# Performance work log

Hardware: AMD Instinct MI355X
Metric: run time of the kernel (lower is better)

Reference implementation:

```python
import jax, jax.numpy as jnp
import numpy as np
from jax import lax

B, CIN, H, W = 16, 256, 64, 64
DP = 512          # displace_planes
COUT = 256        # outplanes
NUM_OFFSET = 64   # displace_planes // BIND_CHAN(8)
K = 5             # DPOOL_SIZE (odd)
EPS = float(np.finfo(np.float32).eps)
BN_EPS = 1e-5
EXP_CLAMP = 88.722835


def conv1x1(x, w, b):
    # x: [B,C,H,W], w: [O,C], b: [O]
    return jnp.einsum('bchw,oc->bohw', x, w) + b[None, :, None, None]


def batchnorm(x, gamma, beta):
    m = x.mean(axis=(0, 2, 3))
    v = x.var(axis=(0, 2, 3))
    inv = lax.rsqrt(v + BN_EPS)
    return (x - m[None, :, None, None]) * (inv * gamma)[None, :, None, None] + beta[None, :, None, None]


def dynamic_pool(x, sigma):
    # per-channel Gaussian depthwise conv in exp space, back to log space
    r = (jnp.arange(K) - K // 2).astype(jnp.float32)
    dissq = r[:, None] ** 2 + r[None, :] ** 2                     # [K,K]
    kern = jnp.exp(-(dissq / 2.0)[None] / (sigma ** 2 + EPS)[:, None, None])  # [C,K,K]
    kern = kern / kern.sum(axis=(1, 2), keepdims=True)
    expx = jnp.exp(jnp.minimum(x, EXP_CLAMP))
    out = lax.conv_general_dilated(
        expx, kern[:, None],                                      # rhs [C,1,K,K]
        window_strides=(1, 1), padding=[(K // 2, K // 2)] * 2,
        dimension_numbers=('NCHW', 'OIHW', 'NCHW'),
        feature_group_count=DP)
    return jnp.log(out + EPS)


def displace(feat, offsets):
    # feat: [B,C,H,W]; offsets: [NUM_OFFSET,2] (dy,dx), each bound to C//NUM_OFFSET channels.
    # Per-channel uniform bilinear shift with zero padding outside the map.
    Bn, C, Hn, Wn = feat.shape
    chan = C // NUM_OFFSET
    dy = jnp.repeat(offsets[:, 0], chan)  # [C]
    dx = jnp.repeat(offsets[:, 1], chan)
    y0 = jnp.floor(dy); x0 = jnp.floor(dx)
    fy = dy - y0; fx = dx - x0            # fractional parts (diff. wrt offsets)
    y0i = y0.astype(jnp.int32); x0i = x0.astype(jnp.int32)
    rows = jnp.arange(Hn); cols = jnp.arange(Wn)

    def one_chan(img, y0c, x0c, fyc, fxc):
        # img: [B,H,W]; shift is separable per row/col since offset is uniform
        def shifted(oy, ox):
            ry = rows + y0c + oy
            rx = cols + x0c + ox
            my = (ry >= 0) & (ry < Hn)
            mx = (rx >= 0) & (rx < Wn)
            g = img[:, jnp.clip(ry, 0, Hn - 1), :][:, :, jnp.clip(rx, 0, Wn - 1)]
            return g * (my[:, None] & mx[None, :]).astype(img.dtype)[None]
        return ((1 - fyc) * (1 - fxc) * shifted(0, 0)
                + (1 - fyc) * fxc * shifted(0, 1)
                + fyc * (1 - fxc) * shifted(1, 0)
                + fyc * fxc * shifted(1, 1))

    return jax.vmap(one_chan, in_axes=(1, 0, 0, 0, 0), out_axes=1)(feat, y0i, x0i, fy, fx)


def attention(x, w, b, gamma, beta):
    a = conv1x1(x, w, b)
    a = batchnorm(a, gamma, beta)
    a = jax.nn.softplus(a)
    # SpaceNormalization: normalize over spatial dims
    return a / a.sum(axis=(2, 3), keepdims=True)


def setup_inputs() -> dict:
    key = jax.random.key(0)
    ks = jax.random.split(key, 6)
    return {
        'x': jax.random.normal(ks[0], (B, CIN, H, W), jnp.float32),
        'pre_w': jax.random.normal(ks[1], (DP, CIN), jnp.float32) / np.sqrt(CIN),
        'pre_b': jnp.zeros((DP,), jnp.float32),
        'sigma': jnp.full((DP,), K / 2 / 2, jnp.float32),
        'offsets': jax.random.normal(ks[2], (NUM_OFFSET, 2), jnp.float32) * 3.0,
        'atten_w': jax.random.normal(ks[3], (DP, CIN), jnp.float32) / np.sqrt(CIN),
        'atten_b': jnp.zeros((DP,), jnp.float32),
        'atten_gamma': jnp.ones((DP,), jnp.float32),
        'atten_beta': jnp.zeros((DP,), jnp.float32),
        'post_w': jax.random.normal(ks[4], (COUT, DP), jnp.float32) / np.sqrt(DP),
        'post_b': jnp.zeros((COUT,), jnp.float32),
        'bn_gamma': jnp.ones((COUT,), jnp.float32),
        'bn_beta': jnp.zeros((COUT,), jnp.float32),
    }


def reference(x, pre_w, pre_b, sigma, offsets, atten_w, atten_b, atten_gamma,
              atten_beta, post_w, post_b, bn_gamma, bn_beta):
    out_pre = conv1x1(x, pre_w, pre_b)                 # [B,DP,H,W]
    out_pre = dynamic_pool(out_pre, sigma)
    out_dis = displace(out_pre, offsets)
    out_atten = attention(x, atten_w, atten_b, atten_gamma, atten_beta)
    out_post = conv1x1(out_atten * out_dis, post_w, post_b)  # [B,COUT,H,W]
    out_skip = x + out_post                            # inplanes==outplanes, stride=1
    return jax.nn.relu(batchnorm(out_skip, bn_gamma, bn_beta))
```

## Files before the change

kernel.cpp:

```cpp
#include <hip/hip_runtime.h>
#include <cmath>

#define NB   16
#define CINC 256
#define DPC  512
#define COUTC 256
#define HWS  4096
#define EPSF 1.1920928955078125e-07f
#define BN_EPS 1e-5f
#define EXP_CLAMP 88.722835f
#define TS 76
#define PS2 66

typedef unsigned int uint32;
typedef unsigned short ushort;
typedef __bf16 bf16x8 __attribute__((ext_vector_type(8)));
typedef float f32x4 __attribute__((ext_vector_type(4)));
typedef unsigned short ushort8 __attribute__((ext_vector_type(8)));

__device__ inline ushort f2bf(float f) {
    __bf16 h = (__bf16)f;
    return __builtin_bit_cast(ushort, h);
}
__device__ inline float bf2f(ushort u) {
    return __builtin_bit_cast(float, (uint32)u << 16);
}
__device__ inline float softplus_fast(float v) {
    return fmaxf(v, 0.f) + __logf(1.f + __expf(-fabsf(v)));
}
__device__ __forceinline__ void gload16(const void* g, void* l) {
    __builtin_amdgcn_global_load_lds(
        (__attribute__((address_space(1))) void*)g,
        (__attribute__((address_space(3))) void*)l, 16, 0, 0);
}

template<int OTOT, int KTOT, bool BF16_OUT, bool ADD_SKIP>
__global__ __launch_bounds__(256) void mfma_gemm_k(
    const ushort* __restrict__ A, const ushort* __restrict__ BT,
    const float* __restrict__ bias1, const float* __restrict__ bias2,
    const float* __restrict__ skip, void* __restrict__ outv) {
    const int hw0 = blockIdx.x * 128;
    const int o0  = blockIdx.y * 128;
    const int b   = blockIdx.z;
    __shared__ ushort As[2 * 128 * 32];
    __shared__ ushort Bs[2 * 128 * 32];
    const int tid  = threadIdx.x;
    const int lane = tid & 63;
    const int w    = tid >> 6;
    const int wm0  = (w >> 1) * 64;
    const int wn0  = (w & 1) * 64;

    f32x4 acc[4][4] = {};

    const ushort* Ab = A + (size_t)o0 * KTOT;
    const ushort* Bb = BT + ((size_t)b * HWS + hw0) * KTOT;
    const int rsub  = lane >> 2;
    const int ksubp = ((lane & 3) ^ ((lane >> 3) & 3)) * 8;

    for (int step = 0; step < KTOT / 64; ++step) {
        const int k0 = step * 64;
#pragma unroll
        for (int h = 0; h < 2; ++h)
#pragma unroll
            for (int i = 0; i < 2; ++i) {
                const int row = w * 32 + i * 16 + rsub;
                gload16(Ab + (size_t)row * KTOT + k0 + h * 32 + ksubp,
                        &As[h * 4096 + (w * 32 + i * 16) * 32]);
                gload16(Bb + (size_t)row * KTOT + k0 + h * 32 + ksubp,
                        &Bs[h * 4096 + (w * 32 + i * 16) * 32]);
            }
        __syncthreads();
        bf16x8 af[2][4], bfr[2][4];
#pragma unroll
        for (int h = 0; h < 2; ++h) {
#pragma unroll
            for (int mi = 0; mi < 4; ++mi) {
                int row = wm0 + mi * 16 + (lane & 15);
                int sl = (lane >> 4) ^ ((row >> 1) & 3);
                af[h][mi] = *reinterpret_cast<const bf16x8*>(As + h * 4096 + row * 32 + sl * 8);
            }
#pragma unroll
            for (int ni = 0; ni < 4; ++ni) {
                int row = wn0 + ni * 16 + (lane & 15);
                int sl = (lane >> 4) ^ ((row >> 1) & 3);
                bfr[h][ni] = *reinterpret_cast<const bf16x8*>(Bs + h * 4096 + row * 32 + sl * 8);
            }
        }
#pragma unroll
        for (int h = 0; h < 2; ++h)
#pragma unroll
            for (int mi = 0; mi < 4; ++mi)
#pragma unroll
                for (int ni = 0; ni < 4; ++ni)
                    acc[mi][ni] = __builtin_amdgcn_mfma_f32_16x16x32_bf16(
                        af[h][mi], bfr[h][ni], acc[mi][ni], 0, 0, 0);
        __syncthreads();
    }

#pragma unroll
    for (int mi = 0; mi < 4; ++mi) {
#pragma unroll
        for (int r = 0; r < 4; ++r) {
            int o = o0 + wm0 + mi * 16 + ((lane >> 4) << 2) + r;
            float bi = (o < 512) ? bias1[o] : bias2[o - 512];
            size_t base = ((size_t)b * OTOT + o) * HWS + hw0 + wn0 + (lane & 15);
            if constexpr (BF16_OUT) {
                ushort* outp = (ushort*)outv;
#pragma unroll
                for (int ni = 0; ni < 4; ++ni)
                    outp[base + ni * 16] = f2bf(acc[mi][ni][r] + bi);
            } else {
                float* outp = (float*)outv;
#pragma unroll
                for (int ni = 0; ni < 4; ++ni) {
                    float v = acc[mi][ni][r] + bi;
                    if constexpr (ADD_SKIP) v += skip[base + ni * 16];
                    outp[base + ni * 16] = v;
                }
            }
        }
    }
}

__global__ __launch_bounds__(256) void castT_k(const float* __restrict__ x,
                                               ushort* __restrict__ xT) {
    const int b = blockIdx.z, c0 = blockIdx.y * 64, hw0 = blockIdx.x * 64;
    __shared__ float tile[64][65];
    const int tid = threadIdx.x;
#pragma unroll
    for (int r = 0; r < 16; ++r) {
        int cl = r * 4 + (tid >> 6), hwl = tid & 63;
        tile[cl][hwl] = x[((size_t)b * CINC + c0 + cl) * HWS + hw0 + hwl];
    }
    __syncthreads();
#pragma unroll
    for (int r = 0; r < 16; ++r) {
        int hwl = r * 4 + (tid >> 6), cl = tid & 63;
        xT[((size_t)b * HWS + hw0 + hwl) * CINC + c0 + cl] = f2bf(tile[cl][hwl]);
    }
}

__global__ __launch_bounds__(256) void cast_k(const float* __restrict__ in,
                                              ushort* __restrict__ out, int n) {
    int i = (blockIdx.x * 256 + threadIdx.x) * 4;
    if (i < n) {
        float4 v = *reinterpret_cast<const float4*>(in + i);
        out[i + 0] = f2bf(v.x); out[i + 1] = f2bf(v.y);
        out[i + 2] = f2bf(v.z); out[i + 3] = f2bf(v.w);
    }
}

__global__ __launch_bounds__(512, 8) void pooldisp_k(ushort* __restrict__ dp,
                                                     const float* __restrict__ sigma,
                                                     const float* __restrict__ offsets) {
    const int bc = blockIdx.x;
    const int b = bc >> 9, c = bc & 511;
    __shared__ float  tmp[68 * TS];
    __shared__ ushort pl[64 * PS2];
    const int tid = threadIdx.x;
    ushort* ip = dp + ((size_t)b * 1024 + c) * HWS;

    float s = sigma[c];
    float inv = 0.5f / (s * s + EPSF);
    float g0 = __expf(-4.f * inv), g1 = __expf(-1.f * inv);
    float gs = g0 + g1 + 1.f + g1 + g0;
    float rnorm = 1.f / (gs * gs);

    {
        int r4 = tid >> 7, col = tid & 127;
        if (col < TS) {
            int row = (r4 < 2) ? r4 : 64 + r4;
            tmp[row * TS + col] = 0.f;
        }
    }
    {
        int hr = tid >> 3, w0 = (tid & 7) * 8;
        const ushort* rp = ip + hr * 64 + w0;
        ushort8 mv = *reinterpret_cast<const ushort8*>(rp);
        float e[12];
        e[0] = (w0 > 0) ? __expf(fminf(bf2f(rp[-2]), EXP_CLAMP)) : 0.f;
        e[1] = (w0 > 0) ? __expf(fminf(bf2f(rp[-1]), EXP_CLAMP)) : 0.f;
#pragma unroll
        for (int q = 0; q < 8; ++q)
            e[2 + q] = __expf(fminf(bf2f(mv[q]), EXP_CLAMP));
        e[10] = (w0 < 56) ? __expf(fminf(bf2f(rp[8]), EXP_CLAMP)) : 0.f;
        e[11] = (w0 < 56) ? __expf(fminf(bf2f(rp[9]), EXP_CLAMP)) : 0.f;
        f32x4 o0, o1;
#pragma unroll
        for (int j = 0; j < 4; ++j) {
            o0[j] = g0 * (e[j] + e[j + 4]) + g1 * (e[j + 1] + e[j + 3]) + e[j + 2];
            o1[j] = g0 * (e[j + 4] + e[j + 8]) + g1 * (e[j + 5] + e[j + 7]) + e[j + 6];
        }
        *reinterpret_cast<f32x4*>(&tmp[(hr + 2) * TS + w0]) = o0;
        *reinterpret_cast<f32x4*>(&tmp[(hr + 2) * TS + w0 + 4]) = o1;
    }
    __syncthreads();

#pragma unroll
    for (int t = 0; t < 2; ++t) {
        int task = tid + t * 512;
        int h = task >> 4, wq = (task & 15) * 4;
        f32x4 t0 = *reinterpret_cast<const f32x4*>(&tmp[(h + 0) * TS + wq]);
        f32x4 t1 = *reinterpret_cast<const f32x4*>(&tmp[(h + 1) * TS + wq]);
        f32x4 t2 = *reinterpret_cast<const f32x4*>(&tmp[(h + 2) * TS + wq]);
        f32x4 t3 = *reinterpret_cast<const f32x4*>(&tmp[(h + 3) * TS + wq]);
        f32x4 t4 = *reinterpret_cast<const f32x4*>(&tmp[(h + 4) * TS + wq]);
        ushort o[4];
#pragma unroll
        for (int j = 0; j < 4; ++j) {
            float v = g0 * (t0[j] + t4[j]) + g1 * (t1[j] + t3[j]) + t2[j];
            o[j] = f2bf(__logf(v * rnorm + EPSF));
        }
        *reinterpret_cast<uint32*>(&pl[h * PS2 + wq]) =
            (uint32)o[0] | ((uint32)o[1] << 16);
        *reinterpret_cast<uint32*>(&pl[h * PS2 + wq + 2]) =
            (uint32)o[2] | ((uint32)o[3] << 16);
    }
    __syncthreads();

    {
        int oi = c >> 3;
        float dy = offsets[oi * 2 + 0];
        float dx = offsets[oi * 2 + 1];
        float y0f = floorf(dy), x0f = floorf(dx);
        float fy = dy - y0f, fx = dx - x0f;
        int y0 = (int)y0f, x0 = (int)x0f;
        float w00 = (1.f - fy) * (1.f - fx), w01 = (1.f - fy) * fx;
        float w10 = fy * (1.f - fx),         w11 = fy * fx;
        int h = tid >> 3, w = (tid & 7) * 8;
        int ry0 = h + y0, ry1 = ry0 + 1;
        bool my0 = (ry0 >= 0) & (ry0 < 64);
        bool my1 = (ry1 >= 0) & (ry1 < 64);
        float e0[9], e1[9];
#pragma unroll
        for (int j = 0; j < 9; ++j) {
            int col = w + x0 + j;
            bool mx = (col >= 0) & (col < 64);
            e0[j] = (my0 & mx) ? bf2f(pl[ry0 * PS2 + col]) : 0.f;
            e1[j] = (my1 & mx) ? bf2f(pl[ry1 * PS2 + col]) : 0.f;
        }
        ushort8 ov;
#pragma unroll
        for (int q = 0; q < 8; ++q)
            ov[q] = f2bf(w00 * e0[q] + w01 * e0[q + 1]
                       + w10 * e1[q] + w11 * e1[q + 1]);
        *reinterpret_cast<ushort8*>(ip + tid * 8) = ov;
    }
}

__global__ __launch_bounds__(1024) void attstats_k(const ushort* __restrict__ dp,
                                                   const float* __restrict__ gamma,
                                                   const float* __restrict__ beta,
                                                   float* __restrict__ scale,
                                                   float* __restrict__ shift,
                                                   float* __restrict__ rsum) {
    const int c = blockIdx.x;
    const int t = threadIdx.x;
    const int wv = t >> 6, lane = t & 63;
    const ushort* p = dp + ((size_t)wv * 1024 + 512 + c) * HWS;

    ushort8 v[8];
    float s = 0.f, s2 = 0.f;
#pragma unroll
    for (int k = 0; k < 8; ++k) {
        v[k] = *reinterpret_cast<const ushort8*>(p + lane * 8 + k * 512);
#pragma unroll
        for (int j = 0; j < 8; ++j) { float f = bf2f(v[k][j]); s += f; s2 += f * f; }
    }
#pragma unroll
    for (int off = 32; off > 0; off >>= 1) {
        s += __shfl_down(s, off, 64);
        s2 += __shfl_down(s2, off, 64);
    }
    __shared__ float t1[16], t2[16], scsh[2];
    if (lane == 0) { t1[wv] = s; t2[wv] = s2; }
    __syncthreads();
    if (t == 0) {
        float S = 0.f, S2 = 0.f;
#pragma unroll
        for (int k = 0; k < 16; ++k) { S += t1[k]; S2 += t2[k]; }
        float n = (float)(NB * HWS);
        float mean = S / n;
        float var = S2 / n - mean * mean;
        float invs = rsqrtf(var + BN_EPS);
        float sc = invs * gamma[c];
        float sh = beta[c] - mean * sc;
        scale[c] = sc; shift[c] = sh;
        scsh[0] = sc; scsh[1] = sh;
    }
    __syncthreads();
    float sc = scsh[0], sh = scsh[1];
    float ps = 0.f;
#pragma unroll
    for (int k = 0; k < 8; ++k)
#pragma unroll
        for (int j = 0; j < 8; ++j)
            ps += softplus_fast(bf2f(v[k][j]) * sc + sh);
#pragma unroll
    for (int off = 32; off > 0; off >>= 1) ps += __shfl_down(ps, off, 64);
    if (lane == 0) rsum[wv * DPC + c] = 1.f / ps;
}

__global__ __launch_bounds__(256) void attmulT_k(const ushort* __restrict__ dp,
                                                 const float* __restrict__ scale,
                                                 const float* __restrict__ shift,
                                                 const float* __restrict__ rsum,
                                                 ushort* __restrict__ mT) {
    const int b = blockIdx.z, c0 = blockIdx.y * 64, hw0 = blockIdx.x * 64;
    __shared__ float tile[64][65];
    const int tid = threadIdx.x;
#pragma unroll
    for (int r = 0; r < 16; ++r) {
        int cl = r * 4 + (tid >> 6), hwl = tid & 63;
        int c = c0 + cl;
        size_t aidx = ((size_t)b * 1024 + 512 + c) * HWS + hw0 + hwl;
        size_t didx = ((size_t)b * 1024 + c) * HWS + hw0 + hwl;
        float a = bf2f(dp[aidx]) * scale[c] + shift[c];
        float m = softplus_fast(a) * rsum[b * DPC + c] * bf2f(dp[didx]);
        tile[cl][hwl] = m;
    }
    __syncthreads();
#pragma unroll
    for (int r = 0; r < 16; ++r) {
        int hwl = r * 4 + (tid >> 6), cl = tid & 63;
        mT[((size_t)b * HWS + hw0 + hwl) * DPC + c0 + cl] = f2bf(tile[cl][hwl]);
    }
}

__global__ __launch_bounds__(1024) void bnstats_k(const float* __restrict__ a,
                                                  const float* __restrict__ gamma,
                                                  const float* __restrict__ beta,
                                                  float* __restrict__ scale,
                                                  float* __restrict__ shift) {
    const int c = blockIdx.x;
    const int t = threadIdx.x;
    const int wv = t >> 6, lane = t & 63;
    const float* p = a + ((size_t)wv * COUTC + c) * HWS;
    float s = 0.f, s2 = 0.f;
#pragma unroll
    for (int k = 0; k < 16; ++k) {
        float4 v = *reinterpret_cast<const float4*>(p + lane * 4 + k * 256);
        s += v.x + v.y + v.z + v.w;
        s2 += v.x * v.x + v.y * v.y + v.z * v.z + v.w * v.w;
    }
#pragma unroll
    for (int off = 32; off > 0; off >>= 1) {
        s += __shfl_down(s, off, 64);
        s2 += __shfl_down(s2, off, 64);
    }
    __shared__ float t1[16], t2[16];
    if (lane == 0) { t1[wv] = s; t2[wv] = s2; }
    __syncthreads();
    if (t == 0) {
        float S = 0.f, S2 = 0.f;
#pragma unroll
        for (int k = 0; k < 16; ++k) { S += t1[k]; S2 += t2[k]; }
        float n = (float)(NB * HWS);
        float mean = S / n;
        float var = S2 / n - mean * mean;
        float invs = rsqrtf(var + BN_EPS);
        float sc = invs * gamma[c];
        scale[c] = sc;
        shift[c] = beta[c] - mean * sc;
    }
}

__global__ __launch_bounds__(256) void final_k(float* __restrict__ out,
                                               const float* __restrict__ scale,
                                               const float* __restrict__ shift) {
    int i = blockIdx.x * 256 + threadIdx.x;
    int c = (i >> 12) & (COUTC - 1);
    float v = out[i] * scale[c] + shift[c];
    out[i] = fmaxf(v, 0.f);
}

extern "C" void kernel_launch(void* const* d_in, const int* in_sizes, int n_in,
                              void* d_out, int out_size, void* d_ws, size_t ws_size,
                              hipStream_t stream) {
    const float* x           = (const float*)d_in[0];
    const float* pre_w       = (const float*)d_in[1];
    const float* pre_b       = (const float*)d_in[2];
    const float* sigma       = (const float*)d_in[3];
    const float* offsets     = (const float*)d_in[4];
    const float* atten_w     = (const float*)d_in[5];
    const float* atten_b     = (const float*)d_in[6];
    const float* atten_gamma = (const float*)d_in[7];
    const float* atten_beta  = (const float*)d_in[8];
    const float* post_w      = (const float*)d_in[9];
    const float* post_b      = (const float*)d_in[10];
    const float* bn_gamma    = (const float*)d_in[11];
    const float* bn_beta     = (const float*)d_in[12];
    float* out = (float*)d_out;

    char* wsb = (char*)d_ws;
    ushort* xT    = (ushort*)(wsb);
    ushort* wbig  = (ushort*)(wsb + ((size_t)32 << 20));
    ushort* wpost = wbig + 1024 * 256;
    float*  stats = (float*)(wsb + ((size_t)33 << 20));
    ushort* dpout = (ushort*)(wsb + ((size_t)34 << 20));
    ushort* mT    = (ushort*)(wsb + ((size_t)162 << 20));

    float* scaleA = stats;
    float* shiftA = stats + 512;
    float* rsum   = stats + 1024;
    float* scale2 = stats + 9216;
    float* shift2 = stats + 9472;

    castT_k<<<dim3(64, 4, NB), 256, 0, stream>>>(x, xT);
    cast_k<<<128, 256, 0, stream>>>(pre_w,   wbig,             DPC * CINC);
    cast_k<<<128, 256, 0, stream>>>(atten_w, wbig + 512 * 256, DPC * CINC);
    cast_k<<<128, 256, 0, stream>>>(post_w,  wpost,            COUTC * DPC);

    mfma_gemm_k<1024, CINC, true, false><<<dim3(32, 8, NB), 256, 0, stream>>>(
        wbig, xT, pre_b, atten_b, nullptr, dpout);
    pooldisp_k<<<NB * DPC, 512, 0, stream>>>(dpout, sigma, offsets);
    attstats_k<<<DPC, 1024, 0, stream>>>(dpout, atten_gamma, atten_beta,
                                         scaleA, shiftA, rsum);
    attmulT_k<<<dim3(64, 8, NB), 256, 0, stream>>>(dpout, scaleA, shiftA, rsum, mT);
    mfma_gemm_k<COUTC, DPC, false, true><<<dim3(32, 2, NB), 256, 0, stream>>>(
        wpost, mT, post_b, post_b, x, out);
    bnstats_k<<<COUTC, 1024, 0, stream>>>(out, bn_gamma, bn_beta, scale2, shift2);
    final_k<<<out_size / 256, 256, 0, stream>>>(out, scale2, shift2);
}
```

Baseline: 288.1 us.

## Fuse BN statistics into post GEMM epilogue and store bf16 intermediate

Result: faster. 276.6 us (-4.0%).

```diff
diff --git a/kernel.cpp b/kernel.cpp
--- a/kernel.cpp
+++ b/kernel.cpp
@@ -34,16 +34,17 @@
         (__attribute__((address_space(3))) void*)l, 16, 0, 0);
 }
 
-template<int OTOT, int KTOT, bool BF16_OUT, bool ADD_SKIP>
+template<int OTOT, int KTOT, bool DUALBIAS, bool PARTIALS>
 __global__ __launch_bounds__(256) void mfma_gemm_k(
     const ushort* __restrict__ A, const ushort* __restrict__ BT,
     const float* __restrict__ bias1, const float* __restrict__ bias2,
-    const float* __restrict__ skip, void* __restrict__ outv) {
+    const float* __restrict__ skip, ushort* __restrict__ outp,
+    float* __restrict__ part_s, float* __restrict__ part_s2) {
     const int hw0 = blockIdx.x * 128;
     const int o0  = blockIdx.y * 128;
     const int b   = blockIdx.z;
-    __shared__ ushort As[2 * 128 * 32];
-    __shared__ ushort Bs[2 * 128 * 32];
+    __shared__ ushort As[2][128 * 32];
+    __shared__ ushort Bs[2][128 * 32];
     const int tid  = threadIdx.x;
     const int lane = tid & 63;
     const int w    = tid >> 6;
@@ -57,67 +58,90 @@
     const int rsub  = lane >> 2;
     const int ksubp = ((lane & 3) ^ ((lane >> 3) & 3)) * 8;
 
-    for (int step = 0; step < KTOT / 64; ++step) {
-        const int k0 = step * 64;
-#pragma unroll
-        for (int h = 0; h < 2; ++h)
-#pragma unroll
-            for (int i = 0; i < 2; ++i) {
-                const int row = w * 32 + i * 16 + rsub;
-                gload16(Ab + (size_t)row * KTOT + k0 + h * 32 + ksubp,
-                        &As[h * 4096 + (w * 32 + i * 16) * 32]);
-                gload16(Bb + (size_t)row * KTOT + k0 + h * 32 + ksubp,
-                        &Bs[h * 4096 + (w * 32 + i * 16) * 32]);
-            }
+    auto stage = [&](int buf, int k0) {
+#pragma unroll
+        for (int i = 0; i < 2; ++i) {
+            const int row = w * 32 + i * 16 + rsub;
+            gload16(Ab + (size_t)row * KTOT + k0 + ksubp, &As[buf][(w * 32 + i * 16) * 32]);
+            gload16(Bb + (size_t)row * KTOT + k0 + ksubp, &Bs[buf][(w * 32 + i * 16) * 32]);
+        }
+    };
+
+    constexpr int NSTEP = KTOT / 32;
+    stage(0, 0);
+    __syncthreads();
+    int cur = 0;
+    for (int step = 0; step < NSTEP; ++step) {
+        if (step + 1 < NSTEP) stage(cur ^ 1, (step + 1) * 32);
+        bf16x8 af[4], bfr[4];
+#pragma unroll
+        for (int mi = 0; mi < 4; ++mi) {
+            int row = wm0 + mi * 16 + (lane & 15);
+            int sl = (lane >> 4) ^ ((row >> 1) & 3);
+            af[mi] = *reinterpret_cast<const bf16x8*>(&As[cur][row * 32 + sl * 8]);
+        }
+#pragma unroll
+        for (int ni = 0; ni < 4; ++ni) {
+            int row = wn0 + ni * 16 + (lane & 15);
+            int sl = (lane >> 4) ^ ((row >> 1) & 3);
+            bfr[ni] = *reinterpret_cast<const bf16x8*>(&Bs[cur][row * 32 + sl * 8]);
+        }
+#pragma unroll
+        for (int mi = 0; mi < 4; ++mi)
+#pragma unroll
+            for (int ni = 0; ni < 4; ++ni)
+                acc[mi][ni] = __builtin_amdgcn_mfma_f32_16x16x32_bf16(
+                    af[mi], bfr[ni], acc[mi][ni], 0, 0, 0);
         __syncthreads();
-        bf16x8 af[2][4], bfr[2][4];
-#pragma unroll
-        for (int h = 0; h < 2; ++h) {
-#pragma unroll
-            for (int mi = 0; mi < 4; ++mi) {
-                int row = wm0 + mi * 16 + (lane & 15);
-                int sl = (lane >> 4) ^ ((row >> 1) & 3);
-                af[h][mi] = *reinterpret_cast<const bf16x8*>(As + h * 4096 + row * 32 + sl * 8);
-            }
+        cur ^= 1;
+    }
+
+    float* pS  = reinterpret_cast<float*>(&As[0][0]);
+    float* pS2 = pS + 256;
+
+#pragma unroll
+    for (int mi = 0; mi < 4; ++mi) {
+#pragma unroll
+        for (int r = 0; r < 4; ++r) {
+            int chL = wm0 + mi * 16 + ((lane >> 4) << 2) + r;
+            int o = o0 + chL;
+            float bi;
+            if constexpr (DUALBIAS) bi = (o < 512) ? bias1[o] : bias2[o - 512];
+            else bi = bias1[o];
+            size_t base = ((size_t)b * OTOT + o) * HWS + hw0 + wn0 + (lane & 15);
+            float s1 = 0.f, s2 = 0.f;
 #pragma unroll
             for (int ni = 0; ni < 4; ++ni) {
-                int row = wn0 + ni * 16 + (lane & 15);
-                int sl = (lane >> 4) ^ ((row >> 1) & 3);
-                bfr[h][ni] = *reinterpret_cast<const bf16x8*>(Bs + h * 4096 + row * 32 + sl * 8);
-            }
-        }
-#pragma unroll
-        for (int h = 0; h < 2; ++h)
-#pragma unroll
-            for (int mi = 0; mi < 4; ++mi)
-#pragma unroll
-                for (int ni = 0; ni < 4; ++ni)
-                    acc[mi][ni] = __builtin_amdgcn_mfma_f32_16x16x32_bf16(
-                        af[h][mi], bfr[h][ni], acc[mi][ni], 0, 0, 0);
-        __syncthreads();
-    }
-
-#pragma unroll
-    for (int mi = 0; mi < 4; ++mi) {
-#pragma unroll
-        for (int r = 0; r < 4; ++r) {
-            int o = o0 + wm0 + mi * 16 + ((lane >> 4) << 2) + r;
-            float bi = (o < 512) ? bias1[o] : bias2[o - 512];
-            size_t base = ((size_t)b * OTOT + o) * HWS + hw0 + wn0 + (lane & 15);
-            if constexpr (BF16_OUT) {
-                ushort* outp = (ushort*)outv;
-#pragma unroll
-                for (int ni = 0; ni < 4; ++ni)
-                    outp[base + ni * 16] = f2bf(acc[mi][ni][r] + bi);
-            } else {
-                float* outp = (float*)outv;
-#pragma unroll
-                for (int ni = 0; ni < 4; ++ni) {
-                    float v = acc[mi][ni][r] + bi;
-                    if constexpr (ADD_SKIP) v += skip[base + ni * 16];
-                    outp[base + ni * 16] = v;
+                float v = acc[mi][ni][r] + bi;
+                if constexpr (PARTIALS) v += skip[base + ni * 16];
+                ushort tb = f2bf(v);
+                outp[base + ni * 16] = tb;
+                if constexpr (PARTIALS) {
+                    float vf = bf2f(tb);
+                    s1 += vf; s2 += vf * vf;
                 }
             }
+            if constexpr (PARTIALS) {
+#pragma unroll
+                for (int off = 1; off <= 8; off <<= 1) {
+                    s1 += __shfl_xor(s1, off, 64);
+                    s2 += __shfl_xor(s2, off, 64);
+                }
+                if ((lane & 15) == 0) {
+                    pS[(w & 1) * 128 + chL]  = s1;
+                    pS2[(w & 1) * 128 + chL] = s2;
+                }
+            }
+        }
+    }
+    if constexpr (PARTIALS) {
+        __syncthreads();
+        if (tid < 128) {
+            int k = blockIdx.x * NB + b;
+            float S  = pS[tid]  + pS[128 + tid];
+            float S2 = pS2[tid] + pS2[128 + tid];
+            part_s[(size_t)(o0 + tid) * 512 + k]  = S;
+            part_s2[(size_t)(o0 + tid) * 512 + k] = S2;
         }
     }
 }
@@ -327,34 +351,27 @@
     }
 }
 
-__global__ __launch_bounds__(1024) void bnstats_k(const float* __restrict__ a,
-                                                  const float* __restrict__ gamma,
-                                                  const float* __restrict__ beta,
-                                                  float* __restrict__ scale,
-                                                  float* __restrict__ shift) {
-    const int c = blockIdx.x;
-    const int t = threadIdx.x;
-    const int wv = t >> 6, lane = t & 63;
-    const float* p = a + ((size_t)wv * COUTC + c) * HWS;
-    float s = 0.f, s2 = 0.f;
-#pragma unroll
-    for (int k = 0; k < 16; ++k) {
-        float4 v = *reinterpret_cast<const float4*>(p + lane * 4 + k * 256);
-        s += v.x + v.y + v.z + v.w;
-        s2 += v.x * v.x + v.y * v.y + v.z * v.z + v.w * v.w;
-    }
+__global__ __launch_bounds__(256) void bnred_k(const float* __restrict__ part_s,
+                                               const float* __restrict__ part_s2,
+                                               const float* __restrict__ gamma,
+                                               const float* __restrict__ beta,
+                                               float* __restrict__ scale,
+                                               float* __restrict__ shift) {
+    const int c = blockIdx.x, t = threadIdx.x;
+    float s  = part_s[(size_t)c * 512 + t]  + part_s[(size_t)c * 512 + 256 + t];
+    float s2 = part_s2[(size_t)c * 512 + t] + part_s2[(size_t)c * 512 + 256 + t];
 #pragma unroll
     for (int off = 32; off > 0; off >>= 1) {
         s += __shfl_down(s, off, 64);
         s2 += __shfl_down(s2, off, 64);
     }
-    __shared__ float t1[16], t2[16];
-    if (lane == 0) { t1[wv] = s; t2[wv] = s2; }
+    __shared__ float t1[4], t2[4];
+    int lane = t & 63, wid = t >> 6;
+    if (lane == 0) { t1[wid] = s; t2[wid] = s2; }
     __syncthreads();
     if (t == 0) {
-        float S = 0.f, S2 = 0.f;
-#pragma unroll
-        for (int k = 0; k < 16; ++k) { S += t1[k]; S2 += t2[k]; }
+        float S = t1[0] + t1[1] + t1[2] + t1[3];
+        float S2 = t2[0] + t2[1] + t2[2] + t2[3];
         float n = (float)(NB * HWS);
         float mean = S / n;
         float var = S2 / n - mean * mean;
@@ -365,13 +382,21 @@
     }
 }
 
-__global__ __launch_bounds__(256) void final_k(float* __restrict__ out,
+__global__ __launch_bounds__(256) void final_k(const ushort* __restrict__ t,
                                                const float* __restrict__ scale,
-                                               const float* __restrict__ shift) {
-    int i = blockIdx.x * 256 + threadIdx.x;
+                                               const float* __restrict__ shift,
+                                               float* __restrict__ out) {
+    int i = (blockIdx.x * 256 + threadIdx.x) * 8;
     int c = (i >> 12) & (COUTC - 1);
-    float v = out[i] * scale[c] + shift[c];
-    out[i] = fmaxf(v, 0.f);
+    float sc = scale[c], sh = shift[c];
+    ushort8 v = *reinterpret_cast<const ushort8*>(t + i);
+    float4 a, b4;
+#pragma unroll
+    for (int j = 0; j < 4; ++j) a[j] = fmaxf(bf2f(v[j]) * sc + sh, 0.f);
+#pragma unroll
+    for (int j = 0; j < 4; ++j) b4[j] = fmaxf(bf2f(v[4 + j]) * sc + sh, 0.f);
+    *reinterpret_cast<float4*>(out + i) = a;
+    *reinterpret_cast<float4*>(out + i + 4) = b4;
 }
 
 extern "C" void kernel_launch(void* const* d_in, const int* in_sizes, int n_in,
@@ -393,12 +418,15 @@
     float* out = (float*)d_out;
 
     char* wsb = (char*)d_ws;
-    ushort* xT    = (ushort*)(wsb);
-    ushort* wbig  = (ushort*)(wsb + ((size_t)32 << 20));
-    ushort* wpost = wbig + 1024 * 256;
-    float*  stats = (float*)(wsb + ((size_t)33 << 20));
-    ushort* dpout = (ushort*)(wsb + ((size_t)34 << 20));
-    ushort* mT    = (ushort*)(wsb + ((size_t)162 << 20));
+    ushort* xT     = (ushort*)(wsb);
+    ushort* wbig   = (ushort*)(wsb + ((size_t)32 << 20));
+    ushort* wpost  = wbig + 1024 * 256;
+    float*  stats  = (float*)(wsb + ((size_t)33 << 20));
+    ushort* dpout  = (ushort*)(wsb + ((size_t)34 << 20));
+    ushort* tbuf   = dpout;
+    ushort* mT     = (ushort*)(wsb + ((size_t)162 << 20));
+    float*  part_s  = (float*)(wsb + ((size_t)226 << 20));
+    float*  part_s2 = part_s + 256 * 512;
 
     float* scaleA = stats;
     float* shiftA = stats + 512;
@@ -412,13 +440,14 @@
     cast_k<<<128, 256, 0, stream>>>(post_w,  wpost,            COUTC * DPC);
 
     mfma_gemm_k<1024, CINC, true, false><<<dim3(32, 8, NB), 256, 0, stream>>>(
-        wbig, xT, pre_b, atten_b, nullptr, dpout);
+        wbig, xT, pre_b, atten_b, nullptr, dpout, nullptr, nullptr);
     pooldisp_k<<<NB * DPC, 512, 0, stream>>>(dpout, sigma, offsets);
     attstats_k<<<DPC, 1024, 0, stream>>>(dpout, atten_gamma, atten_beta,
                                          scaleA, shiftA, rsum);
     attmulT_k<<<dim3(64, 8, NB), 256, 0, stream>>>(dpout, scaleA, shiftA, rsum, mT);
     mfma_gemm_k<COUTC, DPC, false, true><<<dim3(32, 2, NB), 256, 0, stream>>>(
-        wpost, mT, post_b, post_b, x, out);
-    bnstats_k<<<COUTC, 1024, 0, stream>>>(out, bn_gamma, bn_beta, scale2, shift2);
-    final_k<<<out_size / 256, 256, 0, stream>>>(out, scale2, shift2);
-}
+        wpost, mT, post_b, post_b, x, tbuf, part_s, part_s2);
+    bnred_k<<<COUTC, 256, 0, stream>>>(part_s, part_s2, bn_gamma, bn_beta,
+                                       scale2, shift2);
+    final_k<<<(NB * COUTC * HWS) / 2048, 256, 0, stream>>>(tbuf, scale2, shift2, out);
+}
```
